# Kernel tuning notes

Hardware: AMD Instinct MI355X
Metric: run time of the kernel (lower is better)

The kernel has to match this reference:

```python
import jax, jax.numpy as jnp
import numpy as np


def _rms_norm(x, eps=1e-5):
    x32 = x.astype(jnp.float32)
    var = jnp.mean(x32 * x32, axis=-1, keepdims=True)
    return (x32 * jax.lax.rsqrt(var + eps)).astype(x.dtype)


def _rotate_half(x):
    x1, x2 = jnp.split(x, 2, axis=-1)
    return jnp.concatenate([-x2, x1], axis=-1)


def setup_inputs() -> dict:
    key = jax.random.key(0)
    ks = jax.random.split(key, 8)
    B, N, d, dh = 1, 4096, 1024, 64
    inner, k = 2816, 3
    # realistic RoPE cache [N, dh]
    pos = jnp.arange(N, dtype=jnp.float32)[:, None]
    inv = 1.0 / (10000.0 ** (jnp.arange(0, dh, 2, dtype=jnp.float32) / dh))
    ang = pos * inv[None, :]
    ang = jnp.concatenate([ang, ang], axis=-1)
    return {
        'Q_in': jax.random.normal(ks[0], (B, N, d), jnp.float32),
        'cos': jnp.cos(ang),
        'sin': jnp.sin(ang),
        'W_qkv': jax.random.normal(ks[1], (d, 3 * d), jnp.float32) * 0.02,
        'W_o': jax.random.normal(ks[2], (d, d), jnp.float32) * 0.02,
        'W_up': jax.random.normal(ks[3], (d, 2 * inner), jnp.float32) * 0.02,
        'conv_w': jax.random.normal(ks[4], (k, 1, inner), jnp.float32) * 0.1,
        'conv_b': jax.random.normal(ks[5], (inner,), jnp.float32) * 0.01,
        'W_down': jax.random.normal(ks[6], (inner, d), jnp.float32) * 0.02,
    }


def reference(Q_in, cos, sin, W_qkv, W_o, W_up, conv_w, conv_b, W_down):
    B, N, d = Q_in.shape
    H = 16
    dh = d // H
    qkv = (Q_in @ W_qkv).reshape(B, N, 3, H, dh)
    Qp, Kp, Vp = qkv[:, :, 0], qkv[:, :, 1], qkv[:, :, 2]
    # RoPE: cos/sin [N, dh] broadcast over batch and heads
    cb = cos[None, :, None, :]
    sb = sin[None, :, None, :]
    Qp = Qp * cb + _rotate_half(Qp) * sb
    Kp = Kp * cb + _rotate_half(Kp) * sb
    Q = _rms_norm(jnp.transpose(Qp, (0, 2, 1, 3)))  # [B,H,N,dh]
    K = _rms_norm(jnp.transpose(Kp, (0, 2, 1, 3)))
    V = jnp.transpose(Vp, (0, 2, 1, 3))
    # (elu+1)^2 positive-kernel attention (full N x N matrix, as in the source)
    S = jnp.einsum('bhnd,bhmd->bhnm', Q, K) * (dh ** -0.5)
    W = jax.nn.elu(S) + 1.0
    W = W * W  # kernel_power == 2
    Attr = jnp.einsum('bhnm,bhmd->bhnd', W, V)
    C = Attr / (jnp.sum(W, axis=-1, keepdims=True) + 1e-6)
    m = C - V
    m_concat = jnp.transpose(m, (0, 2, 1, 3)).reshape(B, N, d)
    Q_interact = _rms_norm(Q_in + m_concat @ W_o)
    # ConvSwiGLU FFN
    GU = Q_interact @ W_up
    G, U = jnp.split(GU, 2, axis=-1)
    Hf = jax.nn.silu(G) * U  # [B,N,inner]
    Hc = jax.lax.conv_general_dilated(
        Hf, conv_w, window_strides=(1,), padding=[(1, 1)],
        dimension_numbers=('NWC', 'WIO', 'NWC'),
        feature_group_count=Hf.shape[-1])
    Hc = jax.nn.silu(Hc + conv_b)
    return _rms_norm(Q_interact + Hc @ W_down)
```

## Files before the change

### kernel.cpp

```cpp
#include <hip/hip_runtime.h>
#include <hip/hip_bf16.h>
#include <cstdint>

#define N_TOK   4096
#define D_MODEL 1024
#define N_HEAD  16
#define DH      64
#define INNER   2816

typedef __attribute__((ext_vector_type(8))) short bf16x8;
typedef __attribute__((ext_vector_type(4))) float f32x4;
typedef __attribute__((ext_vector_type(8))) unsigned short us8v;
typedef __attribute__((ext_vector_type(4))) unsigned short us4v;

union BF16x8U { bf16x8 v; uint32_t u[4]; };

__device__ __forceinline__ unsigned short f2bf(float x) {
    union { __hip_bfloat16 h; unsigned short u; } c;
    c.h = __float2bfloat16(x);
    return c.u;
}

__device__ __forceinline__ float bf2f(unsigned short u) {
    union { float f; uint32_t i; } c;
    c.i = ((uint32_t)u) << 16;
    return c.f;
}

__device__ __forceinline__ float silu_f(float x) {
    return x / (1.f + __expf(-x));
}

__device__ __forceinline__ void gld16(const unsigned short* g, unsigned short* l) {
    __builtin_amdgcn_global_load_lds(
        (const __attribute__((address_space(1))) void*)g,
        (__attribute__((address_space(3))) void*)l, 16, 0, 0);
}

__global__ __launch_bounds__(256) void cvt_bf16(
    const float* __restrict__ in, unsigned short* __restrict__ out) {
    const size_t i8 = ((size_t)blockIdx.x * 256 + threadIdx.x) * 8;
    float4 a = *reinterpret_cast<const float4*>(&in[i8]);
    float4 b = *reinterpret_cast<const float4*>(&in[i8 + 4]);
    us8v o;
    o[0] = f2bf(a.x); o[1] = f2bf(a.y); o[2] = f2bf(a.z); o[3] = f2bf(a.w);
    o[4] = f2bf(b.x); o[5] = f2bf(b.y); o[6] = f2bf(b.z); o[7] = f2bf(b.w);
    *reinterpret_cast<us8v*>(&out[i8]) = o;
}

__global__ __launch_bounds__(256) void transpose_bf16(
    const float* __restrict__ W, unsigned short* __restrict__ WT,
    int K, int N) {
    __shared__ unsigned short T[64][65];
    const int n0 = blockIdx.x * 64;
    const int k0 = blockIdx.y * 64;
    const int t = threadIdx.x;
#pragma unroll
    for (int i = 0; i < 4; ++i) {
        const int id = i * 256 + t;
        const int r = id >> 4;
        const int c = (id & 15) * 4;
        float4 v = *reinterpret_cast<const float4*>(
            &W[(size_t)(k0 + r) * N + n0 + c]);
        T[c + 0][r] = f2bf(v.x);
        T[c + 1][r] = f2bf(v.y);
        T[c + 2][r] = f2bf(v.z);
        T[c + 3][r] = f2bf(v.w);
    }
    __syncthreads();
#pragma unroll
    for (int i = 0; i < 2; ++i) {
        const int id = i * 256 + t;
        const int n = id >> 3;
        const int c = (id & 7) * 8;
        us8v o;
#pragma unroll
        for (int j = 0; j < 8; ++j) o[j] = T[n][c + j];
        *reinterpret_cast<us8v*>(&WT[(size_t)(n0 + n) * K + k0 + c]) = o;
    }
}

template<int OBF>
__global__ __launch_bounds__(256) void gemm_bf16(
    const unsigned short* __restrict__ A, const unsigned short* __restrict__ Bt,
    void* __restrict__ Cout, int M, int N, int K) {
    __shared__ unsigned short As[128 * 64];
    __shared__ unsigned short Bs[128 * 64];
    const int tid = threadIdx.x;
    const int lane = tid & 63;
    const int w = tid >> 6;
    const int l15 = lane & 15, lg = lane >> 4;
    const int wm = w >> 1, wn = w & 1;
    const int rowBase = blockIdx.y * 128;
    const int colBase = blockIdx.x * 128;

    const int srow = w * 32 + (lane >> 3);
    const int scol = (lane & 7) * 8;
    const unsigned short* Ag = &A[(size_t)(rowBase + srow) * K + scol];
    const unsigned short* Bg = &Bt[(size_t)(colBase + srow) * K + scol];

    f32x4 acc[4][4];
#pragma unroll
    for (int i = 0; i < 4; ++i)
#pragma unroll
        for (int j = 0; j < 4; ++j) acc[i][j] = (f32x4){0.f, 0.f, 0.f, 0.f};

    for (int k0 = 0; k0 < K; k0 += 64) {
#pragma unroll
        for (int j = 0; j < 4; ++j) {
            gld16(Ag + (size_t)j * 8 * K + k0, &As[(w * 32 + j * 8) * 64]);
            gld16(Bg + (size_t)j * 8 * K + k0, &Bs[(w * 32 + j * 8) * 64]);
        }
        __syncthreads();
        bf16x8 af[2][4], bfr[2][4];
#pragma unroll
        for (int kk = 0; kk < 2; ++kk) {
#pragma unroll
            for (int f = 0; f < 4; ++f) {
                af[kk][f] = *reinterpret_cast<const bf16x8*>(
                    &As[(wm * 64 + f * 16 + l15) * 64 + kk * 32 + lg * 8]);
                bfr[kk][f] = *reinterpret_cast<const bf16x8*>(
                    &Bs[(wn * 64 + f * 16 + l15) * 64 + kk * 32 + lg * 8]);
            }
        }
#pragma unroll
        for (int kk = 0; kk < 2; ++kk)
#pragma unroll
            for (int mf = 0; mf < 4; ++mf)
#pragma unroll
                for (int nf = 0; nf < 4; ++nf)
                    acc[mf][nf] = __builtin_amdgcn_mfma_f32_16x16x32_bf16(
                        bfr[kk][nf], af[kk][mf], acc[mf][nf], 0, 0, 0);
        __syncthreads();
    }
#pragma unroll
    for (int mf = 0; mf < 4; ++mf) {
#pragma unroll
        for (int nf = 0; nf < 4; ++nf) {
            const size_t m = rowBase + wm * 64 + mf * 16 + l15;
            const size_t n = colBase + wn * 64 + nf * 16 + lg * 4;
            if (OBF) {
                us4v o;
                o[0] = f2bf(acc[mf][nf][0]); o[1] = f2bf(acc[mf][nf][1]);
                o[2] = f2bf(acc[mf][nf][2]); o[3] = f2bf(acc[mf][nf][3]);
                *reinterpret_cast<us4v*>(
                    &((unsigned short*)Cout)[m * N + n]) = o;
            } else {
                float4 o;
                o.x = acc[mf][nf][0]; o.y = acc[mf][nf][1];
                o.z = acc[mf][nf][2]; o.w = acc[mf][nf][3];
                *reinterpret_cast<float4*>(&((float*)Cout)[m * N + n]) = o;
            }
        }
    }
}

__global__ __launch_bounds__(256) void rope_norm2(
    const float* __restrict__ qkv, const float* __restrict__ cosb,
    const float* __restrict__ sinb, unsigned short* __restrict__ Qb,
    unsigned short* __restrict__ Kb, unsigned short* __restrict__ Vt,
    unsigned short* __restrict__ Vb) {
    const int h = blockIdx.y;
    const int n0 = blockIdx.x * 64;
    const int wv = threadIdx.x >> 6;
    const int lane = threadIdx.x & 63;
    __shared__ unsigned short Vs[64][66];
#pragma unroll 1
    for (int it = 0; it < 16; ++it) {
        const int tn = it * 4 + wv;
        const int n = n0 + tn;
        const float* base = qkv + (size_t)n * (3 * D_MODEL) + h * DH;
        float qv = base[lane];
        float kv = base[D_MODEL + lane];
        float vv = base[2 * D_MODEL + lane];
        const float c = cosb[n * DH + lane];
        const float s = sinb[n * DH + lane];
        const float qp = __shfl(qv, lane ^ 32, 64);
        const float kp = __shfl(kv, lane ^ 32, 64);
        const float sgn = (lane < 32) ? -1.f : 1.f;
        qv = qv * c + sgn * qp * s;
        kv = kv * c + sgn * kp * s;
        float sq = qv * qv, sk = kv * kv;
#pragma unroll
        for (int off = 32; off > 0; off >>= 1) {
            sq += __shfl_xor(sq, off, 64);
            sk += __shfl_xor(sk, off, 64);
        }
        qv *= rsqrtf(sq * (1.f / DH) + 1e-5f) * 0.125f;
        kv *= rsqrtf(sk * (1.f / DH) + 1e-5f);
        const size_t o = ((size_t)h * N_TOK + n) * DH + lane;
        Qb[o] = f2bf(qv);
        Kb[o] = f2bf(kv);
        Vb[o] = f2bf(vv);
        Vs[tn][lane] = f2bf(vv);
    }
    __syncthreads();
    const int d = threadIdx.x >> 2;
    const int c0 = (threadIdx.x & 3) * 16;
    us8v o0, o1;
#pragma unroll
    for (int i = 0; i < 8; ++i) o0[i] = Vs[c0 + i][d];
#pragma unroll
    for (int i = 0; i < 8; ++i) o1[i] = Vs[c0 + 8 + i][d];
    unsigned short* dst = Vt + ((size_t)h * DH + d) * N_TOK + n0 + c0;
    *reinterpret_cast<us8v*>(dst) = o0;
    *reinterpret_cast<us8v*>(dst + 8) = o1;
}

__global__ __launch_bounds__(256, 2) void attn_mfma2(
    const unsigned short* __restrict__ Qb, const unsigned short* __restrict__ Kb,
    const unsigned short* __restrict__ Vt, const unsigned short* __restrict__ Vb,
    unsigned short* __restrict__ Mout) {
    const int B = blockIdx.x;
    const int h = ((B & 7) << 1) | ((B >> 3) & 1);
    const int q0 = (B >> 4) * 64;
    const int lane = threadIdx.x & 63;
    const int wv = threadIdx.x >> 6;
    const int l15 = lane & 15, lg = lane >> 4;
    const unsigned short* Qh = Qb + (size_t)h * N_TOK * DH;
    const unsigned short* Kh = Kb + (size_t)h * N_TOK * DH;
    const unsigned short* Vth = Vt + (size_t)h * DH * N_TOK;

    bf16x8 qf[4][2];
#pragma unroll
    for (int qs = 0; qs < 4; ++qs) {
        const unsigned short* qp = Qh + (size_t)(q0 + qs * 16 + l15) * DH + lg * 8;
        qf[qs][0] = *reinterpret_cast<const bf16x8*>(qp);
        qf[qs][1] = *reinterpret_cast<const bf16x8*>(qp + 32);
    }

    f32x4 ct[4][4];
#pragma unroll
    for (int i = 0; i < 4; ++i)
#pragma unroll
        for (int j = 0; j < 4; ++j) ct[i][j] = (f32x4){0.f, 0.f, 0.f, 0.f};
    float dpart[4] = {0.f, 0.f, 0.f, 0.f};

    const int sA = l15 + ((lg & 1) << 5);
    const int sB = sA + 16;
    const bool hi = (lg & 2) != 0;

#pragma unroll 1
    for (int kt = 0; kt < 16; ++kt) {
        const int k0 = (wv * 16 + kt) * 64;
        const unsigned short* kp = Kh + (size_t)(k0 + l15) * DH + lg * 8;
        bf16x8 kf[4][2];
#pragma unroll
        for (int ks = 0; ks < 4; ++ks) {
            kf[ks][0] = *reinterpret_cast<const bf16x8*>(kp + ks * 16 * DH);
            kf[ks][1] = *reinterpret_cast<const bf16x8*>(kp + ks * 16 * DH + 32);
        }
        const unsigned short* vp = Vth + (size_t)l15 * N_TOK + k0 + lg * 8;
        bf16x8 vf[4][2];
#pragma unroll
        for (int ds = 0; ds < 4; ++ds) {
            vf[ds][0] = *reinterpret_cast<const bf16x8*>(vp + (size_t)ds * 16 * N_TOK);
            vf[ds][1] = *reinterpret_cast<const bf16x8*>(vp + (size_t)ds * 16 * N_TOK + 32);
        }
#pragma unroll
        for (int qs = 0; qs < 4; ++qs) {
            f32x4 st[4];
            __builtin_amdgcn_s_setprio(1);
#pragma unroll
            for (int ks = 0; ks < 4; ++ks) {
                f32x4 z = (f32x4){0.f, 0.f, 0.f, 0.f};
                z = __builtin_amdgcn_mfma_f32_16x16x32_bf16(kf[ks][0], qf[qs][0], z, 0, 0, 0);
                st[ks] = __builtin_amdgcn_mfma_f32_16x16x32_bf16(kf[ks][1], qf[qs][1], z, 0, 0, 0);
            }
            __builtin_amdgcn_s_setprio(0);
            uint32_t wpk[4][2];
#pragma unroll
            for (int ks = 0; ks < 4; ++ks) {
                float w4[4];
#pragma unroll
                for (int r = 0; r < 4; ++r) {
                    const float x = st[ks][r];
                    float e = fmaxf(x, 0.f) + __expf(fminf(x, 0.f));
                    e = e * e;
                    w4[r] = e;
                    dpart[qs] += e;
                }
                wpk[ks][0] = (uint32_t)f2bf(w4[0]) | ((uint32_t)f2bf(w4[1]) << 16);
                wpk[ks][1] = (uint32_t)f2bf(w4[2]) | ((uint32_t)f2bf(w4[3]) << 16);
            }
#pragma unroll
            for (int kh = 0; kh < 2; ++kh) {
                const uint32_t a0 = (uint32_t)__shfl((int)wpk[2 * kh][0], sA, 64);
                const uint32_t a1 = (uint32_t)__shfl((int)wpk[2 * kh][1], sA, 64);
                const uint32_t a2 = (uint32_t)__shfl((int)wpk[2 * kh][0], sB, 64);
                const uint32_t a3 = (uint32_t)__shfl((int)wpk[2 * kh][1], sB, 64);
                const uint32_t b0 = (uint32_t)__shfl((int)wpk[2 * kh + 1][0], sA, 64);
                const uint32_t b1 = (uint32_t)__shfl((int)wpk[2 * kh + 1][1], sA, 64);
                const uint32_t b2 = (uint32_t)__shfl((int)wpk[2 * kh + 1][0], sB, 64);
                const uint32_t b3 = (uint32_t)__shfl((int)wpk[2 * kh + 1][1], sB, 64);
                BF16x8U bb;
                bb.u[0] = hi ? b0 : a0;
                bb.u[1] = hi ? b1 : a1;
                bb.u[2] = hi ? b2 : a2;
                bb.u[3] = hi ? b3 : a3;
                __builtin_amdgcn_s_setprio(1);
#pragma unroll
                for (int ds = 0; ds < 4; ++ds)
                    ct[qs][ds] = __builtin_amdgcn_mfma_f32_16x16x32_bf16(
                        vf[ds][kh], bb.v, ct[qs][ds], 0, 0, 0);
                __builtin_amdgcn_s_setprio(0);
            }
        }
    }

    __shared__ float accs2[2][64][72];
    __shared__ float dens[4][64];
#pragma unroll
    for (int qs = 0; qs < 4; ++qs) {
        float dp = dpart[qs];
        dp += __shfl_xor(dp, 16, 64);
        dp += __shfl_xor(dp, 32, 64);
        if (lg == 0) dens[wv][qs * 16 + l15] = dp;
    }
    if (wv >= 2) {
#pragma unroll
        for (int qs = 0; qs < 4; ++qs)
#pragma unroll
            for (int ds = 0; ds < 4; ++ds)
                *reinterpret_cast<f32x4*>(
                    &accs2[wv - 2][qs * 16 + l15][ds * 16 + lg * 4]) = ct[qs][ds];
    }
    __syncthreads();
    if (wv < 2) {
#pragma unroll
        for (int qs = 0; qs < 4; ++qs)
#pragma unroll
            for (int ds = 0; ds < 4; ++ds)
                ct[qs][ds] += *reinterpret_cast<const f32x4*>(
                    &accs2[wv][qs * 16 + l15][ds * 16 + lg * 4]);
        if (wv == 1) {
#pragma unroll
            for (int qs = 0; qs < 4; ++qs)
#pragma unroll
                for (int ds = 0; ds < 4; ++ds)
                    *reinterpret_cast<f32x4*>(
                        &accs2[1][qs * 16 + l15][ds * 16 + lg * 4]) = ct[qs][ds];
        }
    }
    __syncthreads();
    if (wv == 0) {
#pragma unroll
        for (int qs = 0; qs < 4; ++qs) {
            const int q = qs * 16 + l15;
            const float dnq = 1.f /
                (dens[0][q] + dens[1][q] + dens[2][q] + dens[3][q] + 1e-6f);
            const unsigned short* Vrow = Vb + ((size_t)h * N_TOK + q0 + q) * DH;
            unsigned short* Mrow = Mout + (size_t)(q0 + q) * D_MODEL + h * DH;
#pragma unroll
            for (int ds = 0; ds < 4; ++ds) {
                const int d = ds * 16 + lg * 4;
                const f32x4 s1 = *reinterpret_cast<const f32x4*>(&accs2[1][q][d]);
                const us4v vv = *reinterpret_cast<const us4v*>(&Vrow[d]);
                us4v o;
#pragma unroll
                for (int r = 0; r < 4; ++r)
                    o[r] = f2bf((ct[qs][ds][r] + s1[r]) * dnq - bf2f(vv[r]));
                *reinterpret_cast<us4v*>(&Mrow[d]) = o;
            }
        }
    }
}

template<int WB>
__global__ __launch_bounds__(256) void rms_resid2(
    const float* __restrict__ X, const float* __restrict__ R,
    float* __restrict__ O32, unsigned short* __restrict__ Obf) {
    const int row = blockIdx.x;
    const int tid = threadIdx.x;
    const float4 xv = reinterpret_cast<const float4*>(X + (size_t)row * D_MODEL)[tid];
    const float4 rv = reinterpret_cast<const float4*>(R + (size_t)row * D_MODEL)[tid];
    const float t0 = xv.x + rv.x, t1 = xv.y + rv.y, t2 = xv.z + rv.z, t3 = xv.w + rv.w;
    float ss = t0 * t0 + t1 * t1 + t2 * t2 + t3 * t3;
#pragma unroll
    for (int off = 32; off > 0; off >>= 1) ss += __shfl_xor(ss, off, 64);
    __shared__ float red[4];
    if ((tid & 63) == 0) red[tid >> 6] = ss;
    __syncthreads();
    const float tot = red[0] + red[1] + red[2] + red[3];
    const float rs = rsqrtf(tot * (1.f / D_MODEL) + 1e-5f);
    float4 o;
    o.x = t0 * rs; o.y = t1 * rs; o.z = t2 * rs; o.w = t3 * rs;
    reinterpret_cast<float4*>(O32 + (size_t)row * D_MODEL)[tid] = o;
    if (WB) {
        us4v ob;
        ob[0] = f2bf(o.x); ob[1] = f2bf(o.y); ob[2] = f2bf(o.z); ob[3] = f2bf(o.w);
        *reinterpret_cast<us4v*>(&Obf[(size_t)row * D_MODEL + tid * 4]) = ob;
    }
}

__global__ __launch_bounds__(256) void silu_mul_bf(
    const unsigned short* __restrict__ GU, unsigned short* __restrict__ Hf) {
    const size_t idx = (size_t)blockIdx.x * 256 + threadIdx.x;
    const int c8 = (int)(idx % (INNER / 8)) * 8;
    const int n = (int)(idx / (INNER / 8));
    us8v g = *reinterpret_cast<const us8v*>(&GU[(size_t)n * (2 * INNER) + c8]);
    us8v u = *reinterpret_cast<const us8v*>(&GU[(size_t)n * (2 * INNER) + INNER + c8]);
    us8v o;
#pragma unroll
    for (int j = 0; j < 8; ++j) {
        const float gv = bf2f(g[j]);
        o[j] = f2bf(silu_f(gv) * bf2f(u[j]));
    }
    *reinterpret_cast<us8v*>(&Hf[(size_t)n * INNER + c8]) = o;
}

__global__ __launch_bounds__(256) void dwconv_bf(
    const unsigned short* __restrict__ Hf, const float* __restrict__ W,
    const float* __restrict__ Bv, unsigned short* __restrict__ Hc) {
    const size_t idx = (size_t)blockIdx.x * 256 + threadIdx.x;
    const int c8 = (int)(idx % (INNER / 8)) * 8;
    const int n = (int)(idx / (INNER / 8));
    float a[8];
    {
        float4 b0 = *reinterpret_cast<const float4*>(&Bv[c8]);
        float4 b1 = *reinterpret_cast<const float4*>(&Bv[c8 + 4]);
        a[0] = b0.x; a[1] = b0.y; a[2] = b0.z; a[3] = b0.w;
        a[4] = b1.x; a[5] = b1.y; a[6] = b1.z; a[7] = b1.w;
    }
#pragma unroll
    for (int k = 0; k < 3; ++k) {
        const int nn = n + k - 1;
        if (nn >= 0 && nn < N_TOK) {
            us8v x = *reinterpret_cast<const us8v*>(&Hf[(size_t)nn * INNER + c8]);
            float4 w0 = *reinterpret_cast<const float4*>(&W[(size_t)k * INNER + c8]);
            float4 w1 = *reinterpret_cast<const float4*>(&W[(size_t)k * INNER + c8 + 4]);
            a[0] += bf2f(x[0]) * w0.x; a[1] += bf2f(x[1]) * w0.y;
            a[2] += bf2f(x[2]) * w0.z; a[3] += bf2f(x[3]) * w0.w;
            a[4] += bf2f(x[4]) * w1.x; a[5] += bf2f(x[5]) * w1.y;
            a[6] += bf2f(x[6]) * w1.z; a[7] += bf2f(x[7]) * w1.w;
        }
    }
    us8v o;
#pragma unroll
    for (int j = 0; j < 8; ++j) o[j] = f2bf(silu_f(a[j]));
    *reinterpret_cast<us8v*>(&Hc[(size_t)n * INNER + c8]) = o;
}

extern "C" void kernel_launch(void* const* d_in, const int* in_sizes, int n_in,
                              void* d_out, int out_size, void* d_ws, size_t ws_size,
                              hipStream_t stream) {
    const float* Qin   = (const float*)d_in[0];
    const float* cosb  = (const float*)d_in[1];
    const float* sinb  = (const float*)d_in[2];
    const float* Wqkv  = (const float*)d_in[3];
    const float* Wo    = (const float*)d_in[4];
    const float* Wup   = (const float*)d_in[5];
    const float* convw = (const float*)d_in[6];
    const float* convb = (const float*)d_in[7];
    const float* Wdown = (const float*)d_in[8];
    float* out = (float*)d_out;
    float* ws  = (float*)d_ws;

    unsigned short* WqkvT  = (unsigned short*)(ws);
    unsigned short* WoT    = (unsigned short*)(ws + 1572864);
    unsigned short* WupT   = (unsigned short*)(ws + 2097152);
    unsigned short* WdownT = (unsigned short*)(ws + 4980736);
    unsigned short* Qin_bf = (unsigned short*)(ws + 6422528);
    unsigned short* mcat   = (unsigned short*)(ws + 6422528);
    float*          qkv32  = ws + 8519680;
    float*          wo32   = ws + 8519680;
    unsigned short* GU     = (unsigned short*)(ws + 8519680);
    unsigned short* Hc     = (unsigned short*)(ws + 8519680);
    float*          dn32   = ws + 14286848;
    unsigned short* Qb     = (unsigned short*)(ws + 21102592);
    unsigned short* Kb     = (unsigned short*)(ws + 23199744);
    unsigned short* Vt     = (unsigned short*)(ws + 25296896);
    unsigned short* Vb     = (unsigned short*)(ws + 27394048);
    unsigned short* Hf     = (unsigned short*)(ws + 21102592);
    float*          Qi32   = ws + 29491200;
    unsigned short* Qi_bf  = (unsigned short*)(ws + 33685504);

    const dim3 blk(256);
    cvt_bf16<<<2048, blk, 0, stream>>>(Qin, Qin_bf);
    transpose_bf16<<<dim3(48, 16), blk, 0, stream>>>(Wqkv, WqkvT, 1024, 3072);
    transpose_bf16<<<dim3(16, 16), blk, 0, stream>>>(Wo, WoT, 1024, 1024);
    transpose_bf16<<<dim3(88, 16), blk, 0, stream>>>(Wup, WupT, 1024, 5632);
    transpose_bf16<<<dim3(16, 44), blk, 0, stream>>>(Wdown, WdownT, 2816, 1024);
    gemm_bf16<0><<<dim3(24, 32), blk, 0, stream>>>(
        Qin_bf, WqkvT, qkv32, 4096, 3072, 1024);
    rope_norm2<<<dim3(64, 16), blk, 0, stream>>>(qkv32, cosb, sinb, Qb, Kb, Vt, Vb);
    attn_mfma2<<<1024, blk, 0, stream>>>(Qb, Kb, Vt, Vb, mcat);
    gemm_bf16<0><<<dim3(8, 32), blk, 0, stream>>>(
        mcat, WoT, wo32, 4096, 1024, 1024);
    rms_resid2<1><<<4096, blk, 0, stream>>>(wo32, Qin, Qi32, Qi_bf);
    gemm_bf16<1><<<dim3(44, 32), blk, 0, stream>>>(
        Qi_bf, WupT, GU, 4096, 5632, 1024);
    silu_mul_bf<<<5632, blk, 0, stream>>>(GU, Hf);
    dwconv_bf<<<5632, blk, 0, stream>>>(Hf, convw, convb, Hc);
    gemm_bf16<0><<<dim3(8, 32), blk, 0, stream>>>(
        Hc, WdownT, dn32, 4096, 1024, 2816);
    rms_resid2<0><<<4096, blk, 0, stream>>>(dn32, Qi32, out, nullptr);
}
```

Before: 459.2 us.

## Use 16x16x16 MFMA for PV to drop shuffles, halve query tile, raise occupancy

The attention kernel now runs the W·V product with the 16x16x16 bf16 MFMA, whose operand layout matches the score-MFMA output directly. This removes the cross-lane shuffles and selects that were used to repack weights for the x32 MFMA. The query tile per block drops from 64 to 32 rows, so the grid doubles to 2048 blocks, and launch bounds allow 3 blocks per SM. The trade-off is that K and V tiles are reloaded twice as often per query and V is read with narrower 8-byte loads.

```diff
diff --git a/kernel.cpp b/kernel.cpp
--- a/kernel.cpp
+++ b/kernel.cpp
@@ -9,11 +9,27 @@
 #define INNER   2816
 
 typedef __attribute__((ext_vector_type(8))) short bf16x8;
+typedef __attribute__((ext_vector_type(4))) short bf16x4;
 typedef __attribute__((ext_vector_type(4))) float f32x4;
 typedef __attribute__((ext_vector_type(8))) unsigned short us8v;
 typedef __attribute__((ext_vector_type(4))) unsigned short us4v;
 
 union BF16x8U { bf16x8 v; uint32_t u[4]; };
+union BF16x4U { bf16x4 v; uint32_t u[2]; };
+
+#if defined(__has_builtin)
+#if __has_builtin(__builtin_amdgcn_mfma_f32_16x16x16_bf16)
+#define MFMA16(a, b, c) __builtin_amdgcn_mfma_f32_16x16x16_bf16(a, b, c, 0, 0, 0)
+#define HAVE_MFMA16 1
+#elif __has_builtin(__builtin_amdgcn_mfma_f32_16x16x16bf16_1k)
+#define MFMA16(a, b, c) __builtin_amdgcn_mfma_f32_16x16x16bf16_1k(a, b, c, 0, 0, 0)
+#define HAVE_MFMA16 1
+#else
+#define HAVE_MFMA16 0
+#endif
+#else
+#define HAVE_MFMA16 0
+#endif
 
 __device__ __forceinline__ unsigned short f2bf(float x) {
     union { __hip_bfloat16 h; unsigned short u; } c;
@@ -207,13 +223,13 @@
     *reinterpret_cast<us8v*>(dst + 8) = o1;
 }
 
-__global__ __launch_bounds__(256, 2) void attn_mfma2(
+__global__ __launch_bounds__(256, 3) void attn_mfma2(
     const unsigned short* __restrict__ Qb, const unsigned short* __restrict__ Kb,
     const unsigned short* __restrict__ Vt, const unsigned short* __restrict__ Vb,
     unsigned short* __restrict__ Mout) {
     const int B = blockIdx.x;
     const int h = ((B & 7) << 1) | ((B >> 3) & 1);
-    const int q0 = (B >> 4) * 64;
+    const int q0 = (B >> 4) * 32;
     const int lane = threadIdx.x & 63;
     const int wv = threadIdx.x >> 6;
     const int l15 = lane & 15, lg = lane >> 4;
@@ -221,24 +237,26 @@
     const unsigned short* Kh = Kb + (size_t)h * N_TOK * DH;
     const unsigned short* Vth = Vt + (size_t)h * DH * N_TOK;
 
-    bf16x8 qf[4][2];
-#pragma unroll
-    for (int qs = 0; qs < 4; ++qs) {
+    bf16x8 qf[2][2];
+#pragma unroll
+    for (int qs = 0; qs < 2; ++qs) {
         const unsigned short* qp = Qh + (size_t)(q0 + qs * 16 + l15) * DH + lg * 8;
         qf[qs][0] = *reinterpret_cast<const bf16x8*>(qp);
         qf[qs][1] = *reinterpret_cast<const bf16x8*>(qp + 32);
     }
 
-    f32x4 ct[4][4];
-#pragma unroll
-    for (int i = 0; i < 4; ++i)
+    f32x4 ct[2][4];
+#pragma unroll
+    for (int i = 0; i < 2; ++i)
 #pragma unroll
         for (int j = 0; j < 4; ++j) ct[i][j] = (f32x4){0.f, 0.f, 0.f, 0.f};
-    float dpart[4] = {0.f, 0.f, 0.f, 0.f};
-
+    float dpart[2] = {0.f, 0.f};
+
+#if !HAVE_MFMA16
     const int sA = l15 + ((lg & 1) << 5);
     const int sB = sA + 16;
     const bool hi = (lg & 2) != 0;
+#endif
 
 #pragma unroll 1
     for (int kt = 0; kt < 16; ++kt) {
@@ -250,6 +268,15 @@
             kf[ks][0] = *reinterpret_cast<const bf16x8*>(kp + ks * 16 * DH);
             kf[ks][1] = *reinterpret_cast<const bf16x8*>(kp + ks * 16 * DH + 32);
         }
+#if HAVE_MFMA16
+        bf16x4 vf4[4][4];
+#pragma unroll
+        for (int ds = 0; ds < 4; ++ds)
+#pragma unroll
+            for (int ks = 0; ks < 4; ++ks)
+                vf4[ks][ds] = *reinterpret_cast<const bf16x4*>(
+                    Vth + (size_t)(ds * 16 + l15) * N_TOK + k0 + ks * 16 + lg * 4);
+#else
         const unsigned short* vp = Vth + (size_t)l15 * N_TOK + k0 + lg * 8;
         bf16x8 vf[4][2];
 #pragma unroll
@@ -257,8 +284,9 @@
             vf[ds][0] = *reinterpret_cast<const bf16x8*>(vp + (size_t)ds * 16 * N_TOK);
             vf[ds][1] = *reinterpret_cast<const bf16x8*>(vp + (size_t)ds * 16 * N_TOK + 32);
         }
-#pragma unroll
-        for (int qs = 0; qs < 4; ++qs) {
+#endif
+#pragma unroll
+        for (int qs = 0; qs < 2; ++qs) {
             f32x4 st[4];
             __builtin_amdgcn_s_setprio(1);
 #pragma unroll
@@ -283,6 +311,19 @@
                 wpk[ks][0] = (uint32_t)f2bf(w4[0]) | ((uint32_t)f2bf(w4[1]) << 16);
                 wpk[ks][1] = (uint32_t)f2bf(w4[2]) | ((uint32_t)f2bf(w4[3]) << 16);
             }
+#if HAVE_MFMA16
+            __builtin_amdgcn_s_setprio(1);
+#pragma unroll
+            for (int ks = 0; ks < 4; ++ks) {
+                BF16x4U wu;
+                wu.u[0] = wpk[ks][0];
+                wu.u[1] = wpk[ks][1];
+#pragma unroll
+                for (int ds = 0; ds < 4; ++ds)
+                    ct[qs][ds] = MFMA16(vf4[ks][ds], wu.v, ct[qs][ds]);
+            }
+            __builtin_amdgcn_s_setprio(0);
+#else
 #pragma unroll
             for (int kh = 0; kh < 2; ++kh) {
                 const uint32_t a0 = (uint32_t)__shfl((int)wpk[2 * kh][0], sA, 64);
@@ -305,13 +346,14 @@
                         vf[ds][kh], bb.v, ct[qs][ds], 0, 0, 0);
                 __builtin_amdgcn_s_setprio(0);
             }
-        }
-    }
-
-    __shared__ float accs2[2][64][72];
-    __shared__ float dens[4][64];
-#pragma unroll
-    for (int qs = 0; qs < 4; ++qs) {
+#endif
+        }
+    }
+
+    __shared__ float accs2[2][32][72];
+    __shared__ float dens[4][32];
+#pragma unroll
+    for (int qs = 0; qs < 2; ++qs) {
         float dp = dpart[qs];
         dp += __shfl_xor(dp, 16, 64);
         dp += __shfl_xor(dp, 32, 64);
@@ -319,7 +361,7 @@
     }
     if (wv >= 2) {
 #pragma unroll
-        for (int qs = 0; qs < 4; ++qs)
+        for (int qs = 0; qs < 2; ++qs)
 #pragma unroll
             for (int ds = 0; ds < 4; ++ds)
                 *reinterpret_cast<f32x4*>(
@@ -328,14 +370,14 @@
     __syncthreads();
     if (wv < 2) {
 #pragma unroll
-        for (int qs = 0; qs < 4; ++qs)
+        for (int qs = 0; qs < 2; ++qs)
 #pragma unroll
             for (int ds = 0; ds < 4; ++ds)
                 ct[qs][ds] += *reinterpret_cast<const f32x4*>(
                     &accs2[wv][qs * 16 + l15][ds * 16 + lg * 4]);
         if (wv == 1) {
 #pragma unroll
-            for (int qs = 0; qs < 4; ++qs)
+            for (int qs = 0; qs < 2; ++qs)
 #pragma unroll
                 for (int ds = 0; ds < 4; ++ds)
                     *reinterpret_cast<f32x4*>(
@@ -345,7 +387,7 @@
     __syncthreads();
     if (wv == 0) {
 #pragma unroll
-        for (int qs = 0; qs < 4; ++qs) {
+        for (int qs = 0; qs < 2; ++qs) {
             const int q = qs * 16 + l15;
             const float dnq = 1.f /
                 (dens[0][q] + dens[1][q] + dens[2][q] + dens[3][q] + 1e-6f);
@@ -484,7 +526,7 @@
     gemm_bf16<0><<<dim3(24, 32), blk, 0, stream>>>(
         Qin_bf, WqkvT, qkv32, 4096, 3072, 1024);
     rope_norm2<<<dim3(64, 16), blk, 0, stream>>>(qkv32, cosb, sinb, Qb, Kb, Vt, Vb);
-    attn_mfma2<<<1024, blk, 0, stream>>>(Qb, Kb, Vt, Vb, mcat);
+    attn_mfma2<<<2048, blk, 0, stream>>>(Qb, Kb, Vt, Vb, mcat);
     gemm_bf16<0><<<dim3(8, 32), blk, 0, stream>>>(
         mcat, WoT, wo32, 4096, 1024, 1024);
     rms_resid2<1><<<4096, blk, 0, stream>>>(wo32, Qin, Qi32, Qi_bf);
```

Result: slower. 708.4 us (+54.2%).
